# Optimization experiments

Measured on AMD Instinct MI355X. Metric: run time of the kernel, lower is better.

The kernel has to match this reference:

```python
import jax, jax.numpy as jnp
import numpy as np

D_MODEL = 2048
NUM_HEADS = 16
D_K = D_MODEL // NUM_HEADS
B, S, PAST = 2, 1024, 3072


def setup_inputs() -> dict:
    key = jax.random.key(0)
    ks = jax.random.split(key, 12)
    s = 1.0 / np.sqrt(D_MODEL)
    inp = {
        "x": jax.random.normal(ks[0], (B, S, D_MODEL), dtype=jnp.float32),
        "past_key": jax.random.normal(ks[1], (B, NUM_HEADS, PAST, D_K), dtype=jnp.float32),
        "past_value": jax.random.normal(ks[2], (B, NUM_HEADS, PAST, D_K), dtype=jnp.float32),
        "Wq": jax.random.normal(ks[3], (D_MODEL, D_MODEL), dtype=jnp.float32) * s,
        "bq": jax.random.normal(ks[4], (D_MODEL,), dtype=jnp.float32) * s,
        "Wk": jax.random.normal(ks[5], (D_MODEL, D_MODEL), dtype=jnp.float32) * s,
        "bk": jax.random.normal(ks[6], (D_MODEL,), dtype=jnp.float32) * s,
        "Wv": jax.random.normal(ks[7], (D_MODEL, D_MODEL), dtype=jnp.float32) * s,
        "bv": jax.random.normal(ks[8], (D_MODEL,), dtype=jnp.float32) * s,
        "Wo": jax.random.normal(ks[9], (D_MODEL, D_MODEL), dtype=jnp.float32) * s,
        "bo": jax.random.normal(ks[10], (D_MODEL,), dtype=jnp.float32) * s,
    }
    return inp


def reference(x, past_key, past_value, Wq, bq, Wk, bk, Wv, bv, Wo, bo):
    b, s, _ = x.shape
    # torch nn.Linear: y = x @ W^T + b
    def proj(W, bias):
        y = jnp.einsum('bsd,ed->bse', x, W) + bias
        return y.reshape(b, s, NUM_HEADS, D_K).transpose(0, 2, 1, 3)  # [B,H,S,dk]
    Q = proj(Wq, bq)
    K = proj(Wk, bk)
    V = proj(Wv, bv)
    K = jnp.concatenate([past_key, K], axis=2)   # [B,H,PAST+S,dk]
    V = jnp.concatenate([past_value, V], axis=2)
    scale = 1.0 / np.sqrt(D_K).astype(np.float32)
    scores = jnp.einsum('bhqd,bhkd->bhqk', Q, K) * scale
    attn = jax.nn.softmax(scores, axis=-1)
    out = jnp.einsum('bhqk,bhkd->bhqd', attn, V)          # [B,H,S,dk]
    out = out.transpose(0, 2, 1, 3).reshape(b, s, D_MODEL)
    out = jnp.einsum('bsd,ed->bse', out, Wo) + bo
    return out, K, V
```

## Files before the change

kernel.cpp:

```cpp
#include <hip/hip_runtime.h>
#include <stdint.h>

typedef __bf16 bf16;
typedef __bf16 bf16x4 __attribute__((ext_vector_type(4)));
typedef __bf16 bf16x8 __attribute__((ext_vector_type(8)));
typedef float  f32x4  __attribute__((ext_vector_type(4)));

#define DMODEL 2048
#define NH 16
#define DK 128
#define SS 1024
#define PASTLEN 3072
#define LTOT 4096
#define KVTILES 64
#define NSPLIT 4
#define NT 16

__device__ __forceinline__ void gload16(const void* g, void* l) {
    __builtin_amdgcn_global_load_lds(
        (__attribute__((address_space(1))) void*)(uintptr_t)g,
        (__attribute__((address_space(3))) void*)(uintptr_t)l,
        16, 0, 0);
}

__global__ __launch_bounds__(256) void cvt5_k(
    const float* __restrict__ s0, const float* __restrict__ s1,
    const float* __restrict__ s2, const float* __restrict__ s3,
    const float* __restrict__ s4,
    bf16* __restrict__ d0, bf16* __restrict__ d1, bf16* __restrict__ d2,
    bf16* __restrict__ d3, bf16* __restrict__ d4, int n8)
{
    const float* s; bf16* d;
    switch (blockIdx.y) {
        case 0: s = s0; d = d0; break;
        case 1: s = s1; d = d1; break;
        case 2: s = s2; d = d2; break;
        case 3: s = s3; d = d3; break;
        default: s = s4; d = d4; break;
    }
    int stride = gridDim.x * blockDim.x;
    for (int i = blockIdx.x*blockDim.x + threadIdx.x; i < n8; i += stride) {
        const float4* p = (const float4*)s + (size_t)i*2;
        float4 a = p[0], b = p[1];
        bf16x8 o;
        o[0]=(bf16)a.x; o[1]=(bf16)a.y; o[2]=(bf16)a.z; o[3]=(bf16)a.w;
        o[4]=(bf16)b.x; o[5]=(bf16)b.y; o[6]=(bf16)b.z; o[7]=(bf16)b.w;
        *((bf16x8*)d + i) = o;
    }
}

__global__ __launch_bounds__(256) void gemm_bt(
    const bf16* __restrict__ A,
    const bf16* __restrict__ W0, const bf16* __restrict__ W1, const bf16* __restrict__ W2,
    const float* __restrict__ b0, const float* __restrict__ b1, const float* __restrict__ b2,
    bf16* __restrict__ outQ, float* __restrict__ outK, float* __restrict__ outV,
    float* __restrict__ outO, int mode)
{
    __shared__ __align__(16) bf16 As[128*32];
    __shared__ __align__(16) bf16 Bs[128*32];
    const int tid  = threadIdx.x;
    const int wave = tid >> 6, lane = tid & 63;
    const int l15 = lane & 15, l4 = lane >> 4;
    int which, ntile;
    if (mode == 0) { which = blockIdx.y >> 4; ntile = blockIdx.y & 15; }
    else           { which = 3;               ntile = blockIdx.y; }
    const bf16*  W    = (mode != 0 || which == 0) ? W0 : (which == 1 ? W1 : W2);
    const float* bias = (mode != 0 || which == 0) ? b0 : (which == 1 ? b1 : b2);
    const int m0 = blockIdx.x * 128, n0 = ntile * 128;
    const int wm = wave >> 1, wn = wave & 1;

    f32x4 acc[4][4] = {};

    for (int k0 = 0; k0 < DMODEL; k0 += 32) {
        __syncthreads();
        #pragma unroll
        for (int c = 0; c < 2; ++c) {
            const int base = c*4096 + wave*1024;
            const int byte = base + lane*16;
            const int row  = byte >> 6;
            const int ke   = (byte & 63) >> 1;
            gload16(A + (size_t)(m0+row)*DMODEL + k0 + ke, (char*)As + base);
            gload16(W + (size_t)(n0+row)*DMODEL + k0 + ke, (char*)Bs + base);
        }
        asm volatile("s_waitcnt vmcnt(0)" ::: "memory");
        __syncthreads();
        bf16x8 af[4], bfv[4];
        #pragma unroll
        for (int mf = 0; mf < 4; ++mf)
            af[mf] = *(const bf16x8*)((const char*)As + (wm*64 + mf*16 + l15)*64 + l4*16);
        #pragma unroll
        for (int nf = 0; nf < 4; ++nf)
            bfv[nf] = *(const bf16x8*)((const char*)Bs + (wn*64 + nf*16 + l15)*64 + l4*16);
        #pragma unroll
        for (int mf = 0; mf < 4; ++mf)
            #pragma unroll
            for (int nf = 0; nf < 4; ++nf)
                acc[mf][nf] = __builtin_amdgcn_mfma_f32_16x16x32_bf16(af[mf], bfv[nf], acc[mf][nf], 0, 0, 0);
    }

    float bv4[4];
    #pragma unroll
    for (int nf = 0; nf < 4; ++nf) bv4[nf] = bias[n0 + wn*64 + nf*16 + l15];

    const int rbase = m0 + wm*64 + l4*4;
    const int cbase = n0 + wn*64 + l15;

    if (mode == 1) {
        #pragma unroll
        for (int mf = 0; mf < 4; ++mf)
        #pragma unroll
        for (int nf = 0; nf < 4; ++nf) {
            const int col = cbase + nf*16;
            #pragma unroll
            for (int r = 0; r < 4; ++r) {
                const int row = rbase + mf*16 + r;
                outO[(size_t)row*DMODEL + col] = acc[mf][nf][r] + bv4[nf];
            }
        }
    } else if (which == 0) {
        const float qs = 0.08838834764831845f * 1.4426950408889634f;
        #pragma unroll
        for (int mf = 0; mf < 4; ++mf)
        #pragma unroll
        for (int nf = 0; nf < 4; ++nf) {
            const int col = cbase + nf*16;
            const int h = col >> 7, d = col & 127;
            #pragma unroll
            for (int r = 0; r < 4; ++r) {
                const int row = rbase + mf*16 + r;
                const int b = row >> 10, s = row & 1023;
                outQ[((size_t)(b*NH + h)*SS + s)*DK + d] = (bf16)((acc[mf][nf][r] + bv4[nf]) * qs);
            }
        }
    } else {
        float* dst = (which == 1) ? outK : outV;
        #pragma unroll
        for (int mf = 0; mf < 4; ++mf)
        #pragma unroll
        for (int nf = 0; nf < 4; ++nf) {
            const int col = cbase + nf*16;
            const int h = col >> 7, d = col & 127;
            #pragma unroll
            for (int r = 0; r < 4; ++r) {
                const int row = rbase + mf*16 + r;
                const int b = row >> 10, s = row & 1023;
                dst[((size_t)(b*NH + h)*LTOT + PASTLEN + s)*DK + d] = acc[mf][nf][r] + bv4[nf];
            }
        }
    }
}

__global__ __launch_bounds__(256) void kvprep_k(
    const float* __restrict__ pk, const float* __restrict__ pv,
    float* __restrict__ Kf, float* __restrict__ Vf,
    bf16* __restrict__ Kb, bf16* __restrict__ Vb)
{
    __shared__ float Vt_f[64*132];
    const int tid = threadIdx.x;
    const int tau = blockIdx.x, bh = blockIdx.y;
    const bool past = tau < 48;
    const size_t srcoff = past ? ((size_t)bh*PASTLEN + tau*64)*DK
                               : ((size_t)bh*LTOT    + tau*64)*DK;
    const float* srcK = (past ? pk : Kf) + srcoff;
    const float* srcV = (past ? pv : Vf) + srcoff;
    float* dstKf = Kf + ((size_t)bh*LTOT + tau*64)*DK;
    float* dstVf = Vf + ((size_t)bh*LTOT + tau*64)*DK;
    char* kblob = (char*)Kb + (((size_t)bh*KVTILES + tau) << 14);
    char* vblob = (char*)Vb + (((size_t)bh*KVTILES + tau) << 14);

    #pragma unroll
    for (int i = 0; i < 8; ++i) {
        const int f4 = i*256 + tid;
        const int r  = f4 >> 5;
        const int c8 = f4 & 31;
        float4 k4 = ((const float4*)srcK)[f4];
        float4 v4 = ((const float4*)srcV)[f4];
        if (past) {
            ((float4*)dstKf)[f4] = k4;
            ((float4*)dstVf)[f4] = v4;
        }
        bf16x4 kq; kq[0]=(bf16)k4.x; kq[1]=(bf16)k4.y; kq[2]=(bf16)k4.z; kq[3]=(bf16)k4.w;
        *(bf16x4*)(kblob + r*256 + ((c8*8) ^ ((r&7)<<4))) = kq;
        *(float4*)&Vt_f[r*132 + c8*4] = v4;
    }
    __syncthreads();
    const int d = tid >> 1, half = tid & 1;
    const int dx = (d & 7) << 4;
    #pragma unroll
    for (int jj = 0; jj < 4; ++jj) {
        const int chunk = half*4 + jj;
        bf16x8 o;
        #pragma unroll
        for (int e = 0; e < 8; ++e) {
            const int j  = chunk*8 + e;
            const int oe = (j & 32) + ((j & 4) << 2) + (((j >> 3) & 3) << 2) + (j & 3);
            o[e] = (bf16)Vt_f[oe*132 + d];
        }
        *(bf16x8*)(vblob + d*128 + ((chunk*16) ^ dx)) = o;
    }
}

__global__ __launch_bounds__(512, 2) void attn_k(
    const bf16* __restrict__ Qb,
    const bf16* __restrict__ Kb, const bf16* __restrict__ Vb,
    bf16* __restrict__ Opart, float* __restrict__ Marr, float* __restrict__ Larr)
{
    __shared__ __align__(16) char KL[2][16384];
    __shared__ __align__(16) char VL[2][16384];

    const int tid  = threadIdx.x;
    const int wave = tid >> 6, lane = tid & 63;
    const int l15 = lane & 15, l4 = lane >> 4;
    const int wgid = blockIdx.x;
    const int qt = (wgid >> 3) & 3;
    const int g  = ((wgid >> 5) << 3) | (wgid & 7);
    const int bh = g >> 2, sp = g & 3;
    const int qbase = qt*256 + wave*32;

    bf16x8 qf[2][4];
    #pragma unroll
    for (int qq = 0; qq < 2; ++qq) {
        const bf16* qptr = Qb + ((size_t)bh*SS + qbase + qq*16 + l15)*DK;
        #pragma unroll
        for (int ks = 0; ks < 4; ++ks)
            qf[qq][ks] = *(const bf16x8*)(qptr + ks*32 + l4*8);
    }

    const char* kblobs = (const char*)Kb + (((size_t)bh*KVTILES + sp*NT) << 14);
    const char* vblobs = (const char*)Vb + (((size_t)bh*KVTILES + sp*NT) << 14);
    const int soff = wave*2048;

    bf16x8 ones8;
    #pragma unroll
    for (int e = 0; e < 8; ++e) ones8[e] = (bf16)1.0f;

    float m_run[2];
    f32x4 oacc[2][8];
    f32x4 lacc[2];
    m_run[0] = -1e30f; m_run[1] = -1e30f;
    #pragma unroll
    for (int qq = 0; qq < 2; ++qq) {
        #pragma unroll
        for (int df = 0; df < 8; ++df) oacc[qq][df] = f32x4{0.f,0.f,0.f,0.f};
        lacc[qq] = f32x4{0.f,0.f,0.f,0.f};
    }

    #pragma unroll
    for (int c = 0; c < 2; ++c) {
        gload16(kblobs + soff + c*1024 + lane*16, KL[0] + soff + c*1024);
        gload16(vblobs + soff + c*1024 + lane*16, VL[0] + soff + c*1024);
    }

    for (int t = 0; t < NT; ++t) {
        const int cur = t & 1;
        if (t + 1 < NT) {
            const char* kb = kblobs + ((size_t)(t+1) << 14);
            const char* vb = vblobs + ((size_t)(t+1) << 14);
            #pragma unroll
            for (int c = 0; c < 2; ++c) {
                gload16(kb + soff + c*1024 + lane*16, KL[cur^1] + soff + c*1024);
                gload16(vb + soff + c*1024 + lane*16, VL[cur^1] + soff + c*1024);
            }
            asm volatile("s_waitcnt vmcnt(4)" ::: "memory");
        } else {
            asm volatile("s_waitcnt vmcnt(0)" ::: "memory");
        }
        __builtin_amdgcn_s_barrier();

        const char* Kc = KL[cur];
        const char* Vc = VL[cur];

        f32x4 sa[2][4];
        #pragma unroll
        for (int qq = 0; qq < 2; ++qq)
            #pragma unroll
            for (int nf = 0; nf < 4; ++nf) sa[qq][nf] = f32x4{0.f,0.f,0.f,0.f};
        __builtin_amdgcn_s_setprio(1);
        #pragma unroll
        for (int nf = 0; nf < 4; ++nf) {
            const int krow = nf*16 + l15;
            const int rx = (krow & 7) << 4;
            #pragma unroll
            for (int ks = 0; ks < 4; ++ks) {
                bf16x8 kf = *(const bf16x8*)(Kc + krow*256 + ((ks*64 + l4*16) ^ rx));
                sa[0][nf] = __builtin_amdgcn_mfma_f32_16x16x32_bf16(kf, qf[0][ks], sa[0][nf], 0,0,0);
                sa[1][nf] = __builtin_amdgcn_mfma_f32_16x16x32_bf16(kf, qf[1][ks], sa[1][nf], 0,0,0);
            }
        }
        __builtin_amdgcn_s_setprio(0);

        float mt[2];
        #pragma unroll
        for (int qq = 0; qq < 2; ++qq) {
            float a0 = fmaxf(fmaxf(sa[qq][0][0], sa[qq][0][1]), fmaxf(sa[qq][0][2], sa[qq][0][3]));
            float a1 = fmaxf(fmaxf(sa[qq][1][0], sa[qq][1][1]), fmaxf(sa[qq][1][2], sa[qq][1][3]));
            float a2 = fmaxf(fmaxf(sa[qq][2][0], sa[qq][2][1]), fmaxf(sa[qq][2][2], sa[qq][2][3]));
            float a3 = fmaxf(fmaxf(sa[qq][3][0], sa[qq][3][1]), fmaxf(sa[qq][3][2], sa[qq][3][3]));
            float v = fmaxf(fmaxf(a0, a1), fmaxf(a2, a3));
            v = fmaxf(v, __shfl_xor(v, 16, 64));
            v = fmaxf(v, __shfl_xor(v, 32, 64));
            mt[qq] = v;
        }
        const bool ok = (mt[0] <= m_run[0] + 8.0f) && (mt[1] <= m_run[1] + 8.0f);
        if (!__all(ok)) {
            #pragma unroll
            for (int qq = 0; qq < 2; ++qq) {
                const float mn   = fmaxf(m_run[qq], mt[qq]);
                const float corr = exp2f(m_run[qq] - mn);
                m_run[qq] = mn;
                #pragma unroll
                for (int r = 0; r < 4; ++r) {
                    const float c = __shfl(corr, (lane & 48) | (l4*4 + r), 64);
                    lacc[qq][r] *= c;
                    #pragma unroll
                    for (int df = 0; df < 8; ++df) oacc[qq][df][r] *= c;
                }
            }
        }

        bf16x8 pf[2][2];
        #pragma unroll
        for (int qq = 0; qq < 2; ++qq)
            #pragma unroll
            for (int ks2 = 0; ks2 < 2; ++ks2) {
                bf16x8 v;
                #pragma unroll
                for (int e = 0; e < 8; ++e)
                    v[e] = (bf16)exp2f(sa[qq][ks2*2 + (e >> 2)][e & 3] - m_run[qq]);
                pf[qq][ks2] = v;
            }

        __builtin_amdgcn_s_setprio(1);
        #pragma unroll
        for (int ks2 = 0; ks2 < 2; ++ks2) {
            lacc[0] = __builtin_amdgcn_mfma_f32_16x16x32_bf16(pf[0][ks2], ones8, lacc[0], 0,0,0);
            lacc[1] = __builtin_amdgcn_mfma_f32_16x16x32_bf16(pf[1][ks2], ones8, lacc[1], 0,0,0);
            #pragma unroll
            for (int df = 0; df < 8; ++df) {
                const int d = df*16 + l15;
                bf16x8 vf = *(const bf16x8*)(Vc + d*128 + ((ks2*64 + l4*16) ^ ((d&7)<<4)));
                oacc[0][df] = __builtin_amdgcn_mfma_f32_16x16x32_bf16(pf[0][ks2], vf, oacc[0][df], 0,0,0);
                oacc[1][df] = __builtin_amdgcn_mfma_f32_16x16x32_bf16(pf[1][ks2], vf, oacc[1][df], 0,0,0);
            }
        }
        __builtin_amdgcn_s_setprio(0);

        __builtin_amdgcn_s_barrier();
    }

    bf16* op = Opart + ((size_t)sp*32 + bh)*SS*DK;
    #pragma unroll
    for (int qq = 0; qq < 2; ++qq)
        #pragma unroll
        for (int df = 0; df < 8; ++df)
            #pragma unroll
            for (int r = 0; r < 4; ++r) {
                const int q = qbase + qq*16 + l4*4 + r;
                op[(size_t)q*DK + df*16 + l15] = (bf16)oacc[qq][df][r];
            }
    if (l4 == 0) {
        #pragma unroll
        for (int qq = 0; qq < 2; ++qq)
            Marr[(size_t)sp*32768 + bh*SS + qbase + qq*16 + l15] = m_run[qq];
    }
    if (l15 == 0) {
        #pragma unroll
        for (int qq = 0; qq < 2; ++qq)
            #pragma unroll
            for (int r = 0; r < 4; ++r) {
                const int q = qbase + qq*16 + l4*4 + r;
                Larr[(size_t)sp*32768 + bh*SS + q] = lacc[qq][r];
            }
    }
}

__global__ __launch_bounds__(256) void combine_k(
    const bf16* __restrict__ Opart, const float* __restrict__ Marr,
    const float* __restrict__ Larr, bf16* __restrict__ Ob)
{
    const int gid = blockIdx.x*256 + threadIdx.x;
    const int row = gid >> 4;
    const int c8  = gid & 15;
    const int bh = row >> 10, q = row & 1023;
    float m[NSPLIT], l[NSPLIT];
    #pragma unroll
    for (int s = 0; s < NSPLIT; ++s) {
        m[s] = Marr[(size_t)s*32768 + row];
        l[s] = Larr[(size_t)s*32768 + row];
    }
    float M = m[0];
    #pragma unroll
    for (int s = 1; s < NSPLIT; ++s) M = fmaxf(M, m[s]);
    float w[NSPLIT], den = 0.f;
    #pragma unroll
    for (int s = 0; s < NSPLIT; ++s) { w[s] = exp2f(m[s] - M); den += l[s]*w[s]; }
    const float inv = 1.f / den;
    #pragma unroll
    for (int s = 0; s < NSPLIT; ++s) w[s] *= inv;
    float acc[8] = {};
    #pragma unroll
    for (int s = 0; s < NSPLIT; ++s) {
        bf16x8 p = *(const bf16x8*)(Opart + (size_t)s*4194304 + (size_t)row*DK + c8*8);
        #pragma unroll
        for (int e = 0; e < 8; ++e) acc[e] += (float)p[e]*w[s];
    }
    const int b = bh >> 4, h = bh & 15;
    bf16x8 o;
    #pragma unroll
    for (int e = 0; e < 8; ++e) o[e] = (bf16)acc[e];
    *(bf16x8*)(Ob + ((size_t)(b*SS + q))*DMODEL + h*DK + c8*8) = o;
}

extern "C" void kernel_launch(void* const* d_in, const int* in_sizes, int n_in,
                              void* d_out, int out_size, void* d_ws, size_t ws_size,
                              hipStream_t stream) {
    const float* x  = (const float*)d_in[0];
    const float* pk = (const float*)d_in[1];
    const float* pv = (const float*)d_in[2];
    const float* Wq = (const float*)d_in[3];
    const float* bq = (const float*)d_in[4];
    const float* Wk = (const float*)d_in[5];
    const float* bk = (const float*)d_in[6];
    const float* Wv = (const float*)d_in[7];
    const float* bv = (const float*)d_in[8];
    const float* Wo = (const float*)d_in[9];
    const float* bo = (const float*)d_in[10];

    float* out  = (float*)d_out;
    float* Kout = out + 4194304;
    float* Vout = out + 20971520;

    char* ws = (char*)d_ws;
    bf16* xb    = (bf16*)(ws);
    bf16* Wqb   = (bf16*)(ws + (size_t)8*1024*1024);
    bf16* Wkb   = (bf16*)(ws + (size_t)16*1024*1024);
    bf16* Wvb   = (bf16*)(ws + (size_t)24*1024*1024);
    bf16* Wob   = (bf16*)(ws + (size_t)32*1024*1024);
    bf16* Qb    = (bf16*)(ws + (size_t)40*1024*1024);
    bf16* Ob    = (bf16*)(ws + (size_t)48*1024*1024);
    bf16* Kb    = (bf16*)(ws + (size_t)56*1024*1024);
    bf16* Vb    = (bf16*)(ws + (size_t)88*1024*1024);
    bf16*  Opart = (bf16*)(ws);
    float* Marr  = out;
    float* Larr  = out + 131072;

    cvt5_k<<<dim3(1024, 5), 256, 0, stream>>>(x, Wq, Wk, Wv, Wo,
                                              xb, Wqb, Wkb, Wvb, Wob, 524288);
    gemm_bt<<<dim3(16, 48), 256, 0, stream>>>(xb, Wqb, Wkb, Wvb, bq, bk, bv,
                                              Qb, Kout, Vout, nullptr, 0);
    kvprep_k<<<dim3(64, 32), 256, 0, stream>>>(pk, pv, Kout, Vout, Kb, Vb);
    attn_k<<<512, 512, 0, stream>>>(Qb, Kb, Vb, Opart, Marr, Larr);
    combine_k<<<2048, 256, 0, stream>>>(Opart, Marr, Larr, Ob);
    gemm_bt<<<dim3(16, 16), 256, 0, stream>>>(Ob, Wob, nullptr, nullptr, bo, nullptr, nullptr,
                                              nullptr, nullptr, nullptr, out, 1);
}
```

Before: 290.8 us.

## Fuse KV prep into QKV GEMM and widen attention blocks to 1024 threads

Removes the separate kvprep kernel. Past-KV copying and bf16 blob packing now run in extra blocks of the QKV projection GEMM, and the GEMM epilogue writes the new K/V rows straight into the swizzled bf16 blobs with scalar 2-byte stores. The attention kernel now uses 1024-thread blocks covering 512 queries each, so each wave loads half as much K/V per tile and the grid is halved. This saves one launch and one re-read of the fresh K/V, but adds scattered narrow stores in the GEMM epilogue and lowers occupancy flexibility for attention.

```diff
diff --git a/kernel.cpp b/kernel.cpp
--- a/kernel.cpp
+++ b/kernel.cpp
@@ -54,19 +54,69 @@
     const bf16* __restrict__ W0, const bf16* __restrict__ W1, const bf16* __restrict__ W2,
     const float* __restrict__ b0, const float* __restrict__ b1, const float* __restrict__ b2,
     bf16* __restrict__ outQ, float* __restrict__ outK, float* __restrict__ outV,
-    float* __restrict__ outO, int mode)
+    float* __restrict__ outO,
+    const float* __restrict__ pk, const float* __restrict__ pv,
+    bf16* __restrict__ Kbb, bf16* __restrict__ Vbb, int mode)
 {
-    __shared__ __align__(16) bf16 As[128*32];
-    __shared__ __align__(16) bf16 Bs[128*32];
+    __shared__ __align__(16) char lds[34816];
     const int tid  = threadIdx.x;
+
+    if (mode == 0 && blockIdx.x >= 768) {
+        float* Vt_f = (float*)lds;
+        const int pp  = blockIdx.x - 768;
+        const int tau = pp % 48, bh = pp / 48;
+        const float* srcK = pk + ((size_t)bh*PASTLEN + tau*64)*DK;
+        const float* srcV = pv + ((size_t)bh*PASTLEN + tau*64)*DK;
+        float* dstKf = outK + ((size_t)bh*LTOT + tau*64)*DK;
+        float* dstVf = outV + ((size_t)bh*LTOT + tau*64)*DK;
+        char* kblob = (char*)Kbb + (((size_t)bh*KVTILES + tau) << 14);
+        char* vblob = (char*)Vbb + (((size_t)bh*KVTILES + tau) << 14);
+        #pragma unroll
+        for (int i = 0; i < 8; ++i) {
+            const int f4 = i*256 + tid;
+            const int r  = f4 >> 5;
+            const int c8 = f4 & 31;
+            float4 k4 = ((const float4*)srcK)[f4];
+            float4 v4 = ((const float4*)srcV)[f4];
+            ((float4*)dstKf)[f4] = k4;
+            ((float4*)dstVf)[f4] = v4;
+            bf16x4 kq; kq[0]=(bf16)k4.x; kq[1]=(bf16)k4.y; kq[2]=(bf16)k4.z; kq[3]=(bf16)k4.w;
+            *(bf16x4*)(kblob + r*256 + ((c8*8) ^ ((r&7)<<4))) = kq;
+            *(float4*)&Vt_f[r*132 + c8*4] = v4;
+        }
+        __syncthreads();
+        const int d = tid >> 1, half = tid & 1;
+        const int dx = (d & 7) << 4;
+        #pragma unroll
+        for (int jj = 0; jj < 4; ++jj) {
+            const int chunk = half*4 + jj;
+            bf16x8 o;
+            #pragma unroll
+            for (int e = 0; e < 8; ++e) {
+                const int j  = chunk*8 + e;
+                const int oe = (j & 32) + ((j & 4) << 2) + (((j >> 3) & 3) << 2) + (j & 3);
+                o[e] = (bf16)Vt_f[oe*132 + d];
+            }
+            *(bf16x8*)(vblob + d*128 + ((chunk*16) ^ dx)) = o;
+        }
+        return;
+    }
+
+    bf16* As = (bf16*)lds;
+    bf16* Bs = (bf16*)(lds + 8192);
     const int wave = tid >> 6, lane = tid & 63;
     const int l15 = lane & 15, l4 = lane >> 4;
-    int which, ntile;
-    if (mode == 0) { which = blockIdx.y >> 4; ntile = blockIdx.y & 15; }
-    else           { which = 3;               ntile = blockIdx.y; }
+    int which, ntile, mt;
+    if (mode == 0) {
+        mt = blockIdx.x & 15;
+        const int ny = blockIdx.x >> 4;
+        which = ny >> 4; ntile = ny & 15;
+    } else {
+        mt = blockIdx.x; which = 3; ntile = blockIdx.y;
+    }
     const bf16*  W    = (mode != 0 || which == 0) ? W0 : (which == 1 ? W1 : W2);
     const float* bias = (mode != 0 || which == 0) ? b0 : (which == 1 ? b1 : b2);
-    const int m0 = blockIdx.x * 128, n0 = ntile * 128;
+    const int m0 = mt * 128, n0 = ntile * 128;
     const int wm = wave >> 1, wn = wave & 1;
 
     f32x4 acc[4][4] = {};
@@ -144,63 +194,24 @@
             for (int r = 0; r < 4; ++r) {
                 const int row = rbase + mf*16 + r;
                 const int b = row >> 10, s = row & 1023;
-                dst[((size_t)(b*NH + h)*LTOT + PASTLEN + s)*DK + d] = acc[mf][nf][r] + bv4[nf];
-            }
-        }
-    }
-}
-
-__global__ __launch_bounds__(256) void kvprep_k(
-    const float* __restrict__ pk, const float* __restrict__ pv,
-    float* __restrict__ Kf, float* __restrict__ Vf,
-    bf16* __restrict__ Kb, bf16* __restrict__ Vb)
-{
-    __shared__ float Vt_f[64*132];
-    const int tid = threadIdx.x;
-    const int tau = blockIdx.x, bh = blockIdx.y;
-    const bool past = tau < 48;
-    const size_t srcoff = past ? ((size_t)bh*PASTLEN + tau*64)*DK
-                               : ((size_t)bh*LTOT    + tau*64)*DK;
-    const float* srcK = (past ? pk : Kf) + srcoff;
-    const float* srcV = (past ? pv : Vf) + srcoff;
-    float* dstKf = Kf + ((size_t)bh*LTOT + tau*64)*DK;
-    float* dstVf = Vf + ((size_t)bh*LTOT + tau*64)*DK;
-    char* kblob = (char*)Kb + (((size_t)bh*KVTILES + tau) << 14);
-    char* vblob = (char*)Vb + (((size_t)bh*KVTILES + tau) << 14);
-
-    #pragma unroll
-    for (int i = 0; i < 8; ++i) {
-        const int f4 = i*256 + tid;
-        const int r  = f4 >> 5;
-        const int c8 = f4 & 31;
-        float4 k4 = ((const float4*)srcK)[f4];
-        float4 v4 = ((const float4*)srcV)[f4];
-        if (past) {
-            ((float4*)dstKf)[f4] = k4;
-            ((float4*)dstVf)[f4] = v4;
-        }
-        bf16x4 kq; kq[0]=(bf16)k4.x; kq[1]=(bf16)k4.y; kq[2]=(bf16)k4.z; kq[3]=(bf16)k4.w;
-        *(bf16x4*)(kblob + r*256 + ((c8*8) ^ ((r&7)<<4))) = kq;
-        *(float4*)&Vt_f[r*132 + c8*4] = v4;
-    }
-    __syncthreads();
-    const int d = tid >> 1, half = tid & 1;
-    const int dx = (d & 7) << 4;
-    #pragma unroll
-    for (int jj = 0; jj < 4; ++jj) {
-        const int chunk = half*4 + jj;
-        bf16x8 o;
-        #pragma unroll
-        for (int e = 0; e < 8; ++e) {
-            const int j  = chunk*8 + e;
-            const int oe = (j & 32) + ((j & 4) << 2) + (((j >> 3) & 3) << 2) + (j & 3);
-            o[e] = (bf16)Vt_f[oe*132 + d];
-        }
-        *(bf16x8*)(vblob + d*128 + ((chunk*16) ^ dx)) = o;
-    }
-}
-
-__global__ __launch_bounds__(512, 2) void attn_k(
+                const float val = acc[mf][nf][r] + bv4[nf];
+                dst[((size_t)(b*NH + h)*LTOT + PASTLEN + s)*DK + d] = val;
+                const int tau = 48 + (s >> 6);
+                const int rr  = s & 63;
+                char* blob = (char*)((which == 1) ? Kbb : Vbb)
+                           + (((size_t)(b*NH + h)*KVTILES + tau) << 14);
+                if (which == 1) {
+                    *(bf16*)(blob + rr*256 + ((d*2) ^ ((rr&7)<<4))) = (bf16)val;
+                } else {
+                    const int j = (rr & 32) + ((rr & 16) >> 2) + ((rr & 12) << 1) + (rr & 3);
+                    *(bf16*)(blob + d*128 + ((j*2) ^ ((d&7)<<4))) = (bf16)val;
+                }
+            }
+        }
+    }
+}
+
+__global__ __launch_bounds__(1024, 1) void attn_k(
     const bf16* __restrict__ Qb,
     const bf16* __restrict__ Kb, const bf16* __restrict__ Vb,
     bf16* __restrict__ Opart, float* __restrict__ Marr, float* __restrict__ Larr)
@@ -212,10 +223,10 @@
     const int wave = tid >> 6, lane = tid & 63;
     const int l15 = lane & 15, l4 = lane >> 4;
     const int wgid = blockIdx.x;
-    const int qt = (wgid >> 3) & 3;
-    const int g  = ((wgid >> 5) << 3) | (wgid & 7);
+    const int qt = (wgid >> 3) & 1;
+    const int g  = ((wgid >> 4) << 3) | (wgid & 7);
     const int bh = g >> 2, sp = g & 3;
-    const int qbase = qt*256 + wave*32;
+    const int qbase = qt*512 + wave*32;
 
     bf16x8 qf[2][4];
     #pragma unroll
@@ -228,7 +239,7 @@
 
     const char* kblobs = (const char*)Kb + (((size_t)bh*KVTILES + sp*NT) << 14);
     const char* vblobs = (const char*)Vb + (((size_t)bh*KVTILES + sp*NT) << 14);
-    const int soff = wave*2048;
+    const int soff = wave*1024;
 
     bf16x8 ones8;
     #pragma unroll
@@ -245,23 +256,17 @@
         lacc[qq] = f32x4{0.f,0.f,0.f,0.f};
     }
 
-    #pragma unroll
-    for (int c = 0; c < 2; ++c) {
-        gload16(kblobs + soff + c*1024 + lane*16, KL[0] + soff + c*1024);
-        gload16(vblobs + soff + c*1024 + lane*16, VL[0] + soff + c*1024);
-    }
+    gload16(kblobs + soff + lane*16, KL[0] + soff);
+    gload16(vblobs + soff + lane*16, VL[0] + soff);
 
     for (int t = 0; t < NT; ++t) {
         const int cur = t & 1;
         if (t + 1 < NT) {
             const char* kb = kblobs + ((size_t)(t+1) << 14);
             const char* vb = vblobs + ((size_t)(t+1) << 14);
-            #pragma unroll
-            for (int c = 0; c < 2; ++c) {
-                gload16(kb + soff + c*1024 + lane*16, KL[cur^1] + soff + c*1024);
-                gload16(vb + soff + c*1024 + lane*16, VL[cur^1] + soff + c*1024);
-            }
-            asm volatile("s_waitcnt vmcnt(4)" ::: "memory");
+            gload16(kb + soff + lane*16, KL[cur^1] + soff);
+            gload16(vb + soff + lane*16, VL[cur^1] + soff);
+            asm volatile("s_waitcnt vmcnt(2)" ::: "memory");
         } else {
             asm volatile("s_waitcnt vmcnt(0)" ::: "memory");
         }
@@ -289,7 +294,7 @@
         }
         __builtin_amdgcn_s_setprio(0);
 
-        float mt[2];
+        float mt2[2];
         #pragma unroll
         for (int qq = 0; qq < 2; ++qq) {
             float a0 = fmaxf(fmaxf(sa[qq][0][0], sa[qq][0][1]), fmaxf(sa[qq][0][2], sa[qq][0][3]));
@@ -299,13 +304,13 @@
             float v = fmaxf(fmaxf(a0, a1), fmaxf(a2, a3));
             v = fmaxf(v, __shfl_xor(v, 16, 64));
             v = fmaxf(v, __shfl_xor(v, 32, 64));
-            mt[qq] = v;
-        }
-        const bool ok = (mt[0] <= m_run[0] + 8.0f) && (mt[1] <= m_run[1] + 8.0f);
+            mt2[qq] = v;
+        }
+        const bool ok = (mt2[0] <= m_run[0] + 8.0f) && (mt2[1] <= m_run[1] + 8.0f);
         if (!__all(ok)) {
             #pragma unroll
             for (int qq = 0; qq < 2; ++qq) {
-                const float mn   = fmaxf(m_run[qq], mt[qq]);
+                const float mn   = fmaxf(m_run[qq], mt2[qq]);
                 const float corr = exp2f(m_run[qq] - mn);
                 m_run[qq] = mn;
                 #pragma unroll
@@ -446,11 +451,12 @@
 
     cvt5_k<<<dim3(1024, 5), 256, 0, stream>>>(x, Wq, Wk, Wv, Wo,
                                               xb, Wqb, Wkb, Wvb, Wob, 524288);
-    gemm_bt<<<dim3(16, 48), 256, 0, stream>>>(xb, Wqb, Wkb, Wvb, bq, bk, bv,
-                                              Qb, Kout, Vout, nullptr, 0);
-    kvprep_k<<<dim3(64, 32), 256, 0, stream>>>(pk, pv, Kout, Vout, Kb, Vb);
-    attn_k<<<512, 512, 0, stream>>>(Qb, Kb, Vb, Opart, Marr, Larr);
+    gemm_bt<<<2304, 256, 0, stream>>>(xb, Wqb, Wkb, Wvb, bq, bk, bv,
+                                      Qb, Kout, Vout, nullptr,
+                                      pk, pv, Kb, Vb, 0);
+    attn_k<<<256, 1024, 0, stream>>>(Qb, Kb, Vb, Opart, Marr, Larr);
     combine_k<<<2048, 256, 0, stream>>>(Opart, Marr, Larr, Ob);
     gemm_bt<<<dim3(16, 16), 256, 0, stream>>>(Ob, Wob, nullptr, nullptr, bo, nullptr, nullptr,
-                                              nullptr, nullptr, nullptr, out, 1);
-}
+                                              nullptr, nullptr, nullptr, out,
+                                              nullptr, nullptr, nullptr, nullptr, 1);
+}
```

New measurement: 481.2 us. 1.65x slower.
